# Performance work log

Hardware: AMD Instinct MI355X
Metric: run time of the kernel (lower is better)

The kernel has to match this reference:

```python
import jax, jax.numpy as jnp
import numpy as np

NEG_SLOPE = 0.01  # torch nn.LeakyReLU default

def setup_inputs() -> dict:
    key = jax.random.key(0)
    k1, k2, k3, k4 = jax.random.split(key, 4)
    B, S, D, C = 4, 2048, 1024, 4096
    x = jax.random.normal(k1, (B, S, D), dtype=jnp.float32)
    # _reset_parameters: normal(mean=0, std=0.1)
    atten_emb = jax.random.normal(k2, (C, D), dtype=jnp.float32) * 0.1
    # nn.Linear default init ~ U(-1/sqrt(D), 1/sqrt(D))
    bound = 1.0 / np.sqrt(D)
    W = jax.random.uniform(k3, (C, D), dtype=jnp.float32, minval=-bound, maxval=bound)
    b = jax.random.uniform(k4, (C,), dtype=jnp.float32, minval=-bound, maxval=bound)
    return {"x": x, "atten_emb": atten_emb, "W": W, "b": b}

def reference(x, atten_emb, W, b):
    shape = x.shape
    xf = x.reshape(-1, shape[-1])                      # [N, D]
    # dropout p=0.0 -> identity (eval path)
    scores = jnp.einsum('nd,cd->nc', xf, atten_emb)    # [N, C]
    probs = jax.nn.softmax(scores, axis=-1)
    xf = xf + probs @ atten_emb                        # residual with attended codebook
    y = xf.reshape(shape)
    y = jnp.einsum('...d,cd->...c', y, W) + b          # Linear
    return jnp.where(y >= 0, y, NEG_SLOPE * y)         # LeakyReLU
```

## Files before the change

kernel.cpp:

```cpp
#include <hip/hip_runtime.h>
#include <hip/hip_bf16.h>
#include <stdint.h>

typedef unsigned short u16;
typedef __attribute__((ext_vector_type(8))) short short8;
typedef __attribute__((ext_vector_type(4))) float f32x4;

__device__ inline u16 f2bf(float f) {
  union { float f; uint32_t u; } x; x.f = f;
  uint32_t r = (x.u + 0x7FFFu + ((x.u >> 16) & 1u)) >> 16;
  return (u16)r;
}

__device__ inline void async_load16(const void* g, void* l) {
  __builtin_amdgcn_global_load_lds(
      (const __attribute__((address_space(1))) void*)g,
      (__attribute__((address_space(3))) void*)l, 16, 0, 0);
}

__device__ inline void xcd_remap(int& bx, int& by) {
  int gx = gridDim.x;
  int nwg = gx * gridDim.y;
  int flat = by * gx + bx;
  int swz = (flat & 7) * (nwg >> 3) + (flat >> 3);
  bx = swz % gx;
  by = swz / gx;
}

__global__ __launch_bounds__(256) void f32_to_bf16_k(
    const float* __restrict__ in, u16* __restrict__ out, int n4) {
  int i = blockIdx.x * 256 + threadIdx.x;
  if (i >= n4) return;
  float4 v = reinterpret_cast<const float4*>(in)[i];
  ushort4 o;
  o.x = f2bf(v.x); o.y = f2bf(v.y); o.z = f2bf(v.z); o.w = f2bf(v.w);
  reinterpret_cast<ushort4*>(out)[i] = o;
}

__global__ __launch_bounds__(256) void transpose_f32_bf16_k(
    const float* __restrict__ in, u16* __restrict__ out_t,
    u16* __restrict__ out_nt, int R, int Cc) {
  __shared__ float tile[32][33];
  int tx = threadIdx.x & 31;
  int ty = threadIdx.x >> 5;
  int c = blockIdx.x * 32 + tx;
#pragma unroll
  for (int j = 0; j < 4; j++) {
    int r = blockIdx.y * 32 + ty + j * 8;
    float v = in[(size_t)r * Cc + c];
    tile[ty + j * 8][tx] = v;
    out_nt[(size_t)r * Cc + c] = f2bf(v);
  }
  __syncthreads();
  int rr = blockIdx.y * 32 + tx;
#pragma unroll
  for (int j = 0; j < 4; j++) {
    int cc = blockIdx.x * 32 + ty + j * 8;
    out_t[(size_t)cc * R + rr] = f2bf(tile[tx][ty + j * 8]);
  }
}

__global__ __launch_bounds__(256) void softmax_rows_k(
    const float* __restrict__ S, u16* __restrict__ P, int C) {
  const float4* src = reinterpret_cast<const float4*>(S + (size_t)blockIdx.x * C);
  ushort4* dst = reinterpret_cast<ushort4*>(P + (size_t)blockIdx.x * 2 * C);
  const int t = threadIdx.x;
  float4 v[4];
  float mx = -3.4e38f;
#pragma unroll
  for (int j = 0; j < 4; j++) {
    v[j] = src[j * 256 + t];
    mx = fmaxf(mx, fmaxf(fmaxf(v[j].x, v[j].y), fmaxf(v[j].z, v[j].w)));
  }
#pragma unroll
  for (int i = 1; i < 64; i <<= 1) mx = fmaxf(mx, __shfl_xor(mx, i));
  __shared__ float red[8];
  if ((t & 63) == 0) red[t >> 6] = mx;
  __syncthreads();
  mx = fmaxf(fmaxf(red[0], red[1]), fmaxf(red[2], red[3]));
  float e[16];
  float sum = 0.f;
#pragma unroll
  for (int j = 0; j < 4; j++) {
    e[j * 4 + 0] = __expf(v[j].x - mx);
    e[j * 4 + 1] = __expf(v[j].y - mx);
    e[j * 4 + 2] = __expf(v[j].z - mx);
    e[j * 4 + 3] = __expf(v[j].w - mx);
    sum += (e[j * 4 + 0] + e[j * 4 + 1]) + (e[j * 4 + 2] + e[j * 4 + 3]);
  }
#pragma unroll
  for (int i = 1; i < 64; i <<= 1) sum += __shfl_xor(sum, i);
  if ((t & 63) == 0) red[4 + (t >> 6)] = sum;
  __syncthreads();
  sum = (red[4] + red[5]) + (red[6] + red[7]);
  float inv = 1.0f / sum;
#pragma unroll
  for (int j = 0; j < 4; j++) {
    ushort4 o;
    o.x = f2bf(e[j * 4 + 0] * inv);
    o.y = f2bf(e[j * 4 + 1] * inv);
    o.z = f2bf(e[j * 4 + 2] * inv);
    o.w = f2bf(e[j * 4 + 3] * inv);
    dst[j * 256 + t] = o;
  }
}

template <int EPI>
__global__ __launch_bounds__(512, 2) void gemm_bt256p_k(
    const u16* __restrict__ A, const u16* __restrict__ B,
    int M, int N, int K, int lda,
    float* __restrict__ outF, u16* __restrict__ outBF,
    const float* __restrict__ aux) {
  __shared__ u16 sA[2][256 * 64];
  __shared__ u16 sB[2][256 * 64];

  int bx = blockIdx.x, by = blockIdx.y;
  xcd_remap(bx, by);
  const int mBase = by * 256, nBase = bx * 256;

  const int tid = threadIdx.x;
  const int l = tid & 63;
  const int w = tid >> 6;
  const int wr = w >> 2;
  const int wc = w & 3;
  const int fr = l & 15;
  const int kc4 = l >> 4;

  f32x4 acc[8][4];
#pragma unroll
  for (int m = 0; m < 8; m++)
#pragma unroll
    for (int n = 0; n < 4; n++) acc[m][n] = (f32x4)0.f;

  auto stageA = [&](int buf, int k0, int h) {
#pragma unroll
    for (int q = 0; q < 2; q++) {
      int cc = q * 512 + tid;
      int lr = cc >> 3, cs = cc & 7;
      int gr = (lr & 63) | (h << 6) | ((lr >> 6) << 7);
      int kc = (cs ^ (gr & 7)) << 3;
      async_load16(&A[(size_t)(mBase + gr) * lda + k0 + kc],
                   &sA[buf][gr * 64 + cs * 8]);
    }
  };
  auto stageB = [&](int buf, int k0, int v) {
#pragma unroll
    for (int q = 0; q < 2; q++) {
      int cc = q * 512 + tid;
      int lr = cc >> 3, cs = cc & 7;
      int gr = (lr & 31) | (v << 5) | ((lr >> 5) << 6);
      int kc = (cs ^ (gr & 7)) << 3;
      async_load16(&B[(size_t)(nBase + gr) * K + k0 + kc],
                   &sB[buf][gr * 64 + cs * 8]);
    }
  };

  const int nt = K / 64;
  stageA(0, 0, 0); stageB(0, 0, 0); stageB(0, 0, 1); stageA(0, 0, 1);

  short8 a[4][2], b0[2][2], b1[2][2];

  for (int T = 0; T < nt - 1; ++T) {
    const int buf = T & 1;
    const u16* sa = sA[buf];
    const u16* sb = sB[buf];
    const int k1 = (T + 1) * 64;

    asm volatile("s_waitcnt vmcnt(4)" ::: "memory");
    __builtin_amdgcn_s_barrier();
#pragma unroll
    for (int mm = 0; mm < 4; mm++) {
      int row = wr * 128 + mm * 16 + fr;
#pragma unroll
      for (int kk = 0; kk < 2; kk++)
        a[mm][kk] = *reinterpret_cast<const short8*>(
            &sa[row * 64 + (((kk * 4 + kc4) ^ (row & 7)) << 3)]);
    }
#pragma unroll
    for (int nn = 0; nn < 2; nn++) {
      int row = wc * 64 + nn * 16 + fr;
#pragma unroll
      for (int kk = 0; kk < 2; kk++)
        b0[nn][kk] = *reinterpret_cast<const short8*>(
            &sb[row * 64 + (((kk * 4 + kc4) ^ (row & 7)) << 3)]);
    }
    stageA(buf ^ 1, k1, 0);
    __builtin_amdgcn_s_setprio(1);
#pragma unroll
    for (int mm = 0; mm < 4; mm++)
#pragma unroll
      for (int nn = 0; nn < 2; nn++)
#pragma unroll
        for (int kk = 0; kk < 2; kk++)
          acc[mm][nn] = __builtin_amdgcn_mfma_f32_16x16x32_bf16(
              a[mm][kk], b0[nn][kk], acc[mm][nn], 0, 0, 0);
    __builtin_amdgcn_s_setprio(0);

    asm volatile("s_waitcnt vmcnt(4)" ::: "memory");
    __builtin_amdgcn_s_barrier();
#pragma unroll
    for (int nn = 0; nn < 2; nn++) {
      int row = wc * 64 + 32 + nn * 16 + fr;
#pragma unroll
      for (int kk = 0; kk < 2; kk++)
        b1[nn][kk] = *reinterpret_cast<const short8*>(
            &sb[row * 64 + (((kk * 4 + kc4) ^ (row & 7)) << 3)]);
    }
    stageB(buf ^ 1, k1, 0);
    __builtin_amdgcn_s_setprio(1);
#pragma unroll
    for (int mm = 0; mm < 4; mm++)
#pragma unroll
      for (int nn = 0; nn < 2; nn++)
#pragma unroll
        for (int kk = 0; kk < 2; kk++)
          acc[mm][2 + nn] = __builtin_amdgcn_mfma_f32_16x16x32_bf16(
              a[mm][kk], b1[nn][kk], acc[mm][2 + nn], 0, 0, 0);
    __builtin_amdgcn_s_setprio(0);

    asm volatile("s_waitcnt vmcnt(4)" ::: "memory");
    __builtin_amdgcn_s_barrier();
#pragma unroll
    for (int mm = 0; mm < 4; mm++) {
      int row = wr * 128 + 64 + mm * 16 + fr;
#pragma unroll
      for (int kk = 0; kk < 2; kk++)
        a[mm][kk] = *reinterpret_cast<const short8*>(
            &sa[row * 64 + (((kk * 4 + kc4) ^ (row & 7)) << 3)]);
    }
    stageB(buf ^ 1, k1, 1);
    __builtin_amdgcn_s_setprio(1);
#pragma unroll
    for (int mm = 0; mm < 4; mm++)
#pragma unroll
      for (int nn = 0; nn < 2; nn++)
#pragma unroll
        for (int kk = 0; kk < 2; kk++)
          acc[4 + mm][2 + nn] = __builtin_amdgcn_mfma_f32_16x16x32_bf16(
              a[mm][kk], b1[nn][kk], acc[4 + mm][2 + nn], 0, 0, 0);
    __builtin_amdgcn_s_setprio(0);

    stageA(buf ^ 1, k1, 1);
    __builtin_amdgcn_s_setprio(1);
#pragma unroll
    for (int mm = 0; mm < 4; mm++)
#pragma unroll
      for (int nn = 0; nn < 2; nn++)
#pragma unroll
        for (int kk = 0; kk < 2; kk++)
          acc[4 + mm][nn] = __builtin_amdgcn_mfma_f32_16x16x32_bf16(
              a[mm][kk], b0[nn][kk], acc[4 + mm][nn], 0, 0, 0);
    __builtin_amdgcn_s_setprio(0);
  }

  {
    const int buf = (nt - 1) & 1;
    const u16* sa = sA[buf];
    const u16* sb = sB[buf];

    asm volatile("s_waitcnt vmcnt(4)" ::: "memory");
    __builtin_amdgcn_s_barrier();
#pragma unroll
    for (int mm = 0; mm < 4; mm++) {
      int row = wr * 128 + mm * 16 + fr;
#pragma unroll
      for (int kk = 0; kk < 2; kk++)
        a[mm][kk] = *reinterpret_cast<const short8*>(
            &sa[row * 64 + (((kk * 4 + kc4) ^ (row & 7)) << 3)]);
    }
#pragma unroll
    for (int nn = 0; nn < 2; nn++) {
      int row = wc * 64 + nn * 16 + fr;
#pragma unroll
      for (int kk = 0; kk < 2; kk++)
        b0[nn][kk] = *reinterpret_cast<const short8*>(
            &sb[row * 64 + (((kk * 4 + kc4) ^ (row & 7)) << 3)]);
    }
    __builtin_amdgcn_s_setprio(1);
#pragma unroll
    for (int mm = 0; mm < 4; mm++)
#pragma unroll
      for (int nn = 0; nn < 2; nn++)
#pragma unroll
        for (int kk = 0; kk < 2; kk++)
          acc[mm][nn] = __builtin_amdgcn_mfma_f32_16x16x32_bf16(
              a[mm][kk], b0[nn][kk], acc[mm][nn], 0, 0, 0);
    __builtin_amdgcn_s_setprio(0);

    asm volatile("s_waitcnt vmcnt(2)" ::: "memory");
    __builtin_amdgcn_s_barrier();
#pragma unroll
    for (int nn = 0; nn < 2; nn++) {
      int row = wc * 64 + 32 + nn * 16 + fr;
#pragma unroll
      for (int kk = 0; kk < 2; kk++)
        b1[nn][kk] = *reinterpret_cast<const short8*>(
            &sb[row * 64 + (((kk * 4 + kc4) ^ (row & 7)) << 3)]);
    }
    __builtin_amdgcn_s_setprio(1);
#pragma unroll
    for (int mm = 0; mm < 4; mm++)
#pragma unroll
      for (int nn = 0; nn < 2; nn++)
#pragma unroll
        for (int kk = 0; kk < 2; kk++)
          acc[mm][2 + nn] = __builtin_amdgcn_mfma_f32_16x16x32_bf16(
              a[mm][kk], b1[nn][kk], acc[mm][2 + nn], 0, 0, 0);
    __builtin_amdgcn_s_setprio(0);

    asm volatile("s_waitcnt vmcnt(0)" ::: "memory");
    __builtin_amdgcn_s_barrier();
#pragma unroll
    for (int mm = 0; mm < 4; mm++) {
      int row = wr * 128 + 64 + mm * 16 + fr;
#pragma unroll
      for (int kk = 0; kk < 2; kk++)
        a[mm][kk] = *reinterpret_cast<const short8*>(
            &sa[row * 64 + (((kk * 4 + kc4) ^ (row & 7)) << 3)]);
    }
    __builtin_amdgcn_s_setprio(1);
#pragma unroll
    for (int mm = 0; mm < 4; mm++)
#pragma unroll
      for (int nn = 0; nn < 2; nn++)
#pragma unroll
        for (int kk = 0; kk < 2; kk++)
          acc[4 + mm][2 + nn] = __builtin_amdgcn_mfma_f32_16x16x32_bf16(
              a[mm][kk], b1[nn][kk], acc[4 + mm][2 + nn], 0, 0, 0);
    __builtin_amdgcn_s_setprio(0);

    __builtin_amdgcn_s_setprio(1);
#pragma unroll
    for (int mm = 0; mm < 4; mm++)
#pragma unroll
      for (int nn = 0; nn < 2; nn++)
#pragma unroll
        for (int kk = 0; kk < 2; kk++)
          acc[4 + mm][nn] = __builtin_amdgcn_mfma_f32_16x16x32_bf16(
              a[mm][kk], b0[nn][kk], acc[4 + mm][nn], 0, 0, 0);
    __builtin_amdgcn_s_setprio(0);
  }

#pragma unroll
  for (int m = 0; m < 8; m++) {
#pragma unroll
    for (int n = 0; n < 4; n++) {
      int col = nBase + wc * 64 + n * 16 + fr;
#pragma unroll
      for (int r = 0; r < 4; r++) {
        int row = mBase + wr * 128 + m * 16 + (l >> 4) * 4 + r;
        size_t o = (size_t)row * N + col;
        float v = acc[m][n][r];
        if (EPI == 0) {
          outF[o] = v;
        } else if (EPI == 1) {
          outBF[o] = f2bf(v + aux[o]);
        } else {
          v += aux[col];
          outF[o] = (v >= 0.f) ? v : 0.01f * v;
        }
      }
    }
  }
}

template <int EPI>
__global__ __launch_bounds__(256, 2) void gemm_bt_k(
    const u16* __restrict__ A, const u16* __restrict__ B,
    int M, int N, int K, int lda,
    float* __restrict__ outF, u16* __restrict__ outBF,
    const float* __restrict__ aux) {
  __shared__ u16 sA[4][128 * 32];
  __shared__ u16 sB[4][128 * 32];

  int bx = blockIdx.x, by = blockIdx.y;
  xcd_remap(bx, by);
  const int mBase = by * 128;
  const int nBase = bx * 128;

  const int tid = threadIdx.x;
  const int l = tid & 63;
  const int w = tid >> 6;
  const int wr = w >> 1;
  const int wc = w & 1;
  const int fr = l & 15;
  const int kc4 = l >> 4;

  f32x4 acc[4][4];
#pragma unroll
  for (int m = 0; m < 4; m++)
#pragma unroll
    for (int n = 0; n < 4; n++) acc[m][n] = (f32x4)0.f;

  auto stage = [&](int slot, int k0) {
#pragma unroll
    for (int q = 0; q < 2; q++) {
      int c = q * 256 + tid;
      int row = c >> 2;
      int cs = c & 3;
      int kc = ((cs ^ ((row >> 1) & 3)) << 3);
      async_load16(&A[(size_t)(mBase + row) * lda + k0 + kc], &sA[slot][c * 8]);
      async_load16(&B[(size_t)(nBase + row) * K + k0 + kc], &sB[slot][c * 8]);
    }
  };

  const int nt = K / 32;
  stage(0, 0); stage(1, 32); stage(2, 64); stage(3, 96);

  for (int t = 0; t < nt; ++t) {
    asm volatile("s_waitcnt vmcnt(12)" ::: "memory");
    __builtin_amdgcn_s_barrier();

    const u16* sa = sA[t & 3];
    const u16* sb = sB[t & 3];
    short8 af[4], bf[4];
#pragma unroll
    for (int m = 0; m < 4; m++) {
      int row = wr * 64 + m * 16 + fr;
      af[m] = *reinterpret_cast<const short8*>(
          &sa[row * 32 + ((kc4 ^ ((row >> 1) & 3)) << 3)]);
    }
#pragma unroll
    for (int n = 0; n < 4; n++) {
      int row = wc * 64 + n * 16 + fr;
      bf[n] = *reinterpret_cast<const short8*>(
          &sb[row * 32 + ((kc4 ^ ((row >> 1) & 3)) << 3)]);
    }

    __builtin_amdgcn_s_setprio(1);
#pragma unroll
    for (int m = 0; m < 4; m++)
#pragma unroll
      for (int n = 0; n < 4; n++)
        acc[m][n] = __builtin_amdgcn_mfma_f32_16x16x32_bf16(af[m], bf[n], acc[m][n], 0, 0, 0);
    __builtin_amdgcn_s_setprio(0);

    asm volatile("s_waitcnt lgkmcnt(0)" ::: "memory");
    __builtin_amdgcn_s_barrier();
    if (t + 4 < nt) stage((t + 4) & 3, (t + 4) * 32);
  }

#pragma unroll
  for (int m = 0; m < 4; m++) {
#pragma unroll
    for (int n = 0; n < 4; n++) {
      int col = nBase + wc * 64 + n * 16 + fr;
#pragma unroll
      for (int r = 0; r < 4; r++) {
        int row = mBase + wr * 64 + m * 16 + (l >> 4) * 4 + r;
        size_t o = (size_t)row * N + col;
        float v = acc[m][n][r];
        if (EPI == 0) {
          outF[o] = v;
        } else if (EPI == 1) {
          outBF[o] = f2bf(v + aux[o]);
        } else {
          v += aux[col];
          outF[o] = (v >= 0.f) ? v : 0.01f * v;
        }
      }
    }
  }
}

extern "C" void kernel_launch(void* const* d_in, const int* in_sizes, int n_in,
                              void* d_out, int out_size, void* d_ws, size_t ws_size,
                              hipStream_t stream) {
  const float* x = (const float*)d_in[0];
  const float* E = (const float*)d_in[1];
  const float* W = (const float*)d_in[2];
  const float* bias = (const float*)d_in[3];

  const int C = in_sizes[3];
  const int D = in_sizes[1] / C;
  const int Mrows = in_sizes[0] / D;

  char* p = (char*)d_ws;
  u16* xbf = (u16*)p;   p += (size_t)Mrows * D * 2;
  u16* Ebf = (u16*)p;   p += (size_t)C * D * 2;
  u16* Etbf = (u16*)p;  p += (size_t)C * D * 2;
  u16* Wbf = (u16*)p;   p += (size_t)C * D * 2;
  u16* x2bf = (u16*)p;  p += (size_t)Mrows * D * 2;
  float* scores = (float*)p;
  u16* probs = (u16*)scores + C;

  {
    int n4 = Mrows * D / 4;
    f32_to_bf16_k<<<(n4 + 255) / 256, 256, 0, stream>>>(x, xbf, n4);
  }
  {
    int n4 = C * D / 4;
    f32_to_bf16_k<<<(n4 + 255) / 256, 256, 0, stream>>>(W, Wbf, n4);
  }
  transpose_f32_bf16_k<<<dim3(D / 32, C / 32), 256, 0, stream>>>(E, Etbf, Ebf, C, D);

  gemm_bt256p_k<0><<<dim3(C / 256, Mrows / 256), 512, 0, stream>>>(
      xbf, Ebf, Mrows, C, D, D, scores, nullptr, nullptr);

  softmax_rows_k<<<Mrows, 256, 0, stream>>>(scores, probs, C);

  gemm_bt_k<1><<<dim3(D / 128, Mrows / 128), 256, 0, stream>>>(
      probs, Etbf, Mrows, D, C, 2 * C, nullptr, x2bf, x);

  gemm_bt256p_k<2><<<dim3(C / 256, Mrows / 256), 512, 0, stream>>>(
      x2bf, Wbf, Mrows, C, D, D, (float*)d_out, nullptr, bias);
}
```

Before: 438.6 us.

## Fuse prep conversions into one kernel and retile probs@E GEMM to 256x128

```diff
diff --git a/kernel.cpp b/kernel.cpp
--- a/kernel.cpp
+++ b/kernel.cpp
@@ -27,36 +27,58 @@
   by = swz / gx;
 }
 
-__global__ __launch_bounds__(256) void f32_to_bf16_k(
-    const float* __restrict__ in, u16* __restrict__ out, int n4) {
-  int i = blockIdx.x * 256 + threadIdx.x;
-  if (i >= n4) return;
-  float4 v = reinterpret_cast<const float4*>(in)[i];
-  ushort4 o;
-  o.x = f2bf(v.x); o.y = f2bf(v.y); o.z = f2bf(v.z); o.w = f2bf(v.w);
-  reinterpret_cast<ushort4*>(out)[i] = o;
-}
-
-__global__ __launch_bounds__(256) void transpose_f32_bf16_k(
-    const float* __restrict__ in, u16* __restrict__ out_t,
-    u16* __restrict__ out_nt, int R, int Cc) {
+__global__ __launch_bounds__(256) void prep_k(
+    const float* __restrict__ x, u16* __restrict__ xbf, int n4x, int nbx,
+    const float* __restrict__ W, u16* __restrict__ Wbf, int n4w, int nbw,
+    const float* __restrict__ E, u16* __restrict__ Ebf, u16* __restrict__ Etbf,
+    int R, int Cc) {
   __shared__ float tile[32][33];
-  int tx = threadIdx.x & 31;
-  int ty = threadIdx.x >> 5;
-  int c = blockIdx.x * 32 + tx;
-#pragma unroll
-  for (int j = 0; j < 4; j++) {
-    int r = blockIdx.y * 32 + ty + j * 8;
-    float v = in[(size_t)r * Cc + c];
-    tile[ty + j * 8][tx] = v;
-    out_nt[(size_t)r * Cc + c] = f2bf(v);
-  }
-  __syncthreads();
-  int rr = blockIdx.y * 32 + tx;
-#pragma unroll
-  for (int j = 0; j < 4; j++) {
-    int cc = blockIdx.x * 32 + ty + j * 8;
-    out_t[(size_t)cc * R + rr] = f2bf(tile[tx][ty + j * 8]);
+  const int b = blockIdx.x;
+  const int t = threadIdx.x;
+  if (b < nbx) {
+#pragma unroll
+    for (int j = 0; j < 4; j++) {
+      int i = b * 1024 + j * 256 + t;
+      if (i < n4x) {
+        float4 v = reinterpret_cast<const float4*>(x)[i];
+        ushort4 o;
+        o.x = f2bf(v.x); o.y = f2bf(v.y); o.z = f2bf(v.z); o.w = f2bf(v.w);
+        reinterpret_cast<ushort4*>(xbf)[i] = o;
+      }
+    }
+  } else if (b < nbx + nbw) {
+    int bb = b - nbx;
+#pragma unroll
+    for (int j = 0; j < 4; j++) {
+      int i = bb * 1024 + j * 256 + t;
+      if (i < n4w) {
+        float4 v = reinterpret_cast<const float4*>(W)[i];
+        ushort4 o;
+        o.x = f2bf(v.x); o.y = f2bf(v.y); o.z = f2bf(v.z); o.w = f2bf(v.w);
+        reinterpret_cast<ushort4*>(Wbf)[i] = o;
+      }
+    }
+  } else {
+    int bb = b - nbx - nbw;
+    int gbx = bb % (Cc / 32);
+    int gby = bb / (Cc / 32);
+    int tx = t & 31;
+    int ty = t >> 5;
+    int c = gbx * 32 + tx;
+#pragma unroll
+    for (int j = 0; j < 4; j++) {
+      int r = gby * 32 + ty + j * 8;
+      float v = E[(size_t)r * Cc + c];
+      tile[ty + j * 8][tx] = v;
+      Ebf[(size_t)r * Cc + c] = f2bf(v);
+    }
+    __syncthreads();
+    int rr = gby * 32 + tx;
+#pragma unroll
+    for (int j = 0; j < 4; j++) {
+      int cc = gbx * 32 + ty + j * 8;
+      Etbf[(size_t)cc * R + rr] = f2bf(tile[tx][ty + j * 8]);
+    }
   }
 }
 
@@ -353,8 +375,6 @@
         float v = acc[m][n][r];
         if (EPI == 0) {
           outF[o] = v;
-        } else if (EPI == 1) {
-          outBF[o] = f2bf(v + aux[o]);
         } else {
           v += aux[col];
           outF[o] = (v >= 0.f) ? v : 0.01f * v;
@@ -364,100 +384,184 @@
   }
 }
 
-template <int EPI>
-__global__ __launch_bounds__(256, 2) void gemm_bt_k(
+__global__ __launch_bounds__(512, 2) void gemm2_k(
     const u16* __restrict__ A, const u16* __restrict__ B,
     int M, int N, int K, int lda,
-    float* __restrict__ outF, u16* __restrict__ outBF,
-    const float* __restrict__ aux) {
-  __shared__ u16 sA[4][128 * 32];
-  __shared__ u16 sB[4][128 * 32];
+    u16* __restrict__ outBF, const float* __restrict__ aux) {
+  __shared__ u16 sA[2][256 * 64];
+  __shared__ u16 sB[2][128 * 64];
 
   int bx = blockIdx.x, by = blockIdx.y;
   xcd_remap(bx, by);
-  const int mBase = by * 128;
-  const int nBase = bx * 128;
+  const int mBase = by * 256, nBase = bx * 128;
 
   const int tid = threadIdx.x;
   const int l = tid & 63;
   const int w = tid >> 6;
-  const int wr = w >> 1;
-  const int wc = w & 1;
+  const int wr = w >> 2;
+  const int wc = w & 3;
   const int fr = l & 15;
   const int kc4 = l >> 4;
 
-  f32x4 acc[4][4];
-#pragma unroll
-  for (int m = 0; m < 4; m++)
-#pragma unroll
-    for (int n = 0; n < 4; n++) acc[m][n] = (f32x4)0.f;
-
-  auto stage = [&](int slot, int k0) {
+  f32x4 acc[8][2];
+#pragma unroll
+  for (int m = 0; m < 8; m++)
+#pragma unroll
+    for (int n = 0; n < 2; n++) acc[m][n] = (f32x4)0.f;
+
+  auto stageA = [&](int buf, int k0, int h) {
 #pragma unroll
     for (int q = 0; q < 2; q++) {
-      int c = q * 256 + tid;
-      int row = c >> 2;
-      int cs = c & 3;
-      int kc = ((cs ^ ((row >> 1) & 3)) << 3);
-      async_load16(&A[(size_t)(mBase + row) * lda + k0 + kc], &sA[slot][c * 8]);
-      async_load16(&B[(size_t)(nBase + row) * K + k0 + kc], &sB[slot][c * 8]);
+      int cc = q * 512 + tid;
+      int lr = cc >> 3, cs = cc & 7;
+      int gr = (lr & 63) | (h << 6) | ((lr >> 6) << 7);
+      int kc = (cs ^ (gr & 7)) << 3;
+      async_load16(&A[(size_t)(mBase + gr) * lda + k0 + kc],
+                   &sA[buf][gr * 64 + cs * 8]);
     }
   };
-
-  const int nt = K / 32;
-  stage(0, 0); stage(1, 32); stage(2, 64); stage(3, 96);
-
-  for (int t = 0; t < nt; ++t) {
-    asm volatile("s_waitcnt vmcnt(12)" ::: "memory");
-    __builtin_amdgcn_s_barrier();
-
-    const u16* sa = sA[t & 3];
-    const u16* sb = sB[t & 3];
-    short8 af[4], bf[4];
-#pragma unroll
-    for (int m = 0; m < 4; m++) {
-      int row = wr * 64 + m * 16 + fr;
-      af[m] = *reinterpret_cast<const short8*>(
-          &sa[row * 32 + ((kc4 ^ ((row >> 1) & 3)) << 3)]);
-    }
-#pragma unroll
-    for (int n = 0; n < 4; n++) {
-      int row = wc * 64 + n * 16 + fr;
-      bf[n] = *reinterpret_cast<const short8*>(
-          &sb[row * 32 + ((kc4 ^ ((row >> 1) & 3)) << 3)]);
-    }
-
-    __builtin_amdgcn_s_setprio(1);
-#pragma unroll
-    for (int m = 0; m < 4; m++)
-#pragma unroll
-      for (int n = 0; n < 4; n++)
-        acc[m][n] = __builtin_amdgcn_mfma_f32_16x16x32_bf16(af[m], bf[n], acc[m][n], 0, 0, 0);
-    __builtin_amdgcn_s_setprio(0);
-
-    asm volatile("s_waitcnt lgkmcnt(0)" ::: "memory");
-    __builtin_amdgcn_s_barrier();
-    if (t + 4 < nt) stage((t + 4) & 3, (t + 4) * 32);
-  }
-
-#pragma unroll
-  for (int m = 0; m < 4; m++) {
-#pragma unroll
-    for (int n = 0; n < 4; n++) {
-      int col = nBase + wc * 64 + n * 16 + fr;
+  auto stageB = [&](int buf, int k0) {
+#pragma unroll
+    for (int q = 0; q < 2; q++) {
+      int cc = q * 512 + tid;
+      int gr = cc >> 3, cs = cc & 7;
+      int kc = (cs ^ (gr & 7)) << 3;
+      async_load16(&B[(size_t)(nBase + gr) * K + k0 + kc],
+                   &sB[buf][gr * 64 + cs * 8]);
+    }
+  };
+
+  const int nt = K / 64;
+  stageA(0, 0, 0); stageB(0, 0); stageA(0, 0, 1);
+
+  short8 a[4][2], b[2][2];
+
+  for (int T = 0; T < nt - 1; ++T) {
+    const int buf = T & 1;
+    const u16* sa = sA[buf];
+    const u16* sb = sB[buf];
+    const int k1 = (T + 1) * 64;
+
+    asm volatile("s_waitcnt vmcnt(2)" ::: "memory");
+    __builtin_amdgcn_s_barrier();
+#pragma unroll
+    for (int mm = 0; mm < 4; mm++) {
+      int row = wr * 128 + mm * 16 + fr;
+#pragma unroll
+      for (int kk = 0; kk < 2; kk++)
+        a[mm][kk] = *reinterpret_cast<const short8*>(
+            &sa[row * 64 + (((kk * 4 + kc4) ^ (row & 7)) << 3)]);
+    }
+#pragma unroll
+    for (int nn = 0; nn < 2; nn++) {
+      int row = wc * 32 + nn * 16 + fr;
+#pragma unroll
+      for (int kk = 0; kk < 2; kk++)
+        b[nn][kk] = *reinterpret_cast<const short8*>(
+            &sb[row * 64 + (((kk * 4 + kc4) ^ (row & 7)) << 3)]);
+    }
+    stageA(buf ^ 1, k1, 0);
+    __builtin_amdgcn_s_setprio(1);
+#pragma unroll
+    for (int mm = 0; mm < 4; mm++)
+#pragma unroll
+      for (int nn = 0; nn < 2; nn++)
+#pragma unroll
+        for (int kk = 0; kk < 2; kk++)
+          acc[mm][nn] = __builtin_amdgcn_mfma_f32_16x16x32_bf16(
+              a[mm][kk], b[nn][kk], acc[mm][nn], 0, 0, 0);
+    __builtin_amdgcn_s_setprio(0);
+
+    asm volatile("s_waitcnt vmcnt(2)" ::: "memory");
+    __builtin_amdgcn_s_barrier();
+#pragma unroll
+    for (int mm = 0; mm < 4; mm++) {
+      int row = wr * 128 + 64 + mm * 16 + fr;
+#pragma unroll
+      for (int kk = 0; kk < 2; kk++)
+        a[mm][kk] = *reinterpret_cast<const short8*>(
+            &sa[row * 64 + (((kk * 4 + kc4) ^ (row & 7)) << 3)]);
+    }
+    stageB(buf ^ 1, k1);
+    stageA(buf ^ 1, k1, 1);
+    __builtin_amdgcn_s_setprio(1);
+#pragma unroll
+    for (int mm = 0; mm < 4; mm++)
+#pragma unroll
+      for (int nn = 0; nn < 2; nn++)
+#pragma unroll
+        for (int kk = 0; kk < 2; kk++)
+          acc[4 + mm][nn] = __builtin_amdgcn_mfma_f32_16x16x32_bf16(
+              a[mm][kk], b[nn][kk], acc[4 + mm][nn], 0, 0, 0);
+    __builtin_amdgcn_s_setprio(0);
+  }
+
+  {
+    const int buf = (nt - 1) & 1;
+    const u16* sa = sA[buf];
+    const u16* sb = sB[buf];
+
+    asm volatile("s_waitcnt vmcnt(2)" ::: "memory");
+    __builtin_amdgcn_s_barrier();
+#pragma unroll
+    for (int mm = 0; mm < 4; mm++) {
+      int row = wr * 128 + mm * 16 + fr;
+#pragma unroll
+      for (int kk = 0; kk < 2; kk++)
+        a[mm][kk] = *reinterpret_cast<const short8*>(
+            &sa[row * 64 + (((kk * 4 + kc4) ^ (row & 7)) << 3)]);
+    }
+#pragma unroll
+    for (int nn = 0; nn < 2; nn++) {
+      int row = wc * 32 + nn * 16 + fr;
+#pragma unroll
+      for (int kk = 0; kk < 2; kk++)
+        b[nn][kk] = *reinterpret_cast<const short8*>(
+            &sb[row * 64 + (((kk * 4 + kc4) ^ (row & 7)) << 3)]);
+    }
+    __builtin_amdgcn_s_setprio(1);
+#pragma unroll
+    for (int mm = 0; mm < 4; mm++)
+#pragma unroll
+      for (int nn = 0; nn < 2; nn++)
+#pragma unroll
+        for (int kk = 0; kk < 2; kk++)
+          acc[mm][nn] = __builtin_amdgcn_mfma_f32_16x16x32_bf16(
+              a[mm][kk], b[nn][kk], acc[mm][nn], 0, 0, 0);
+    __builtin_amdgcn_s_setprio(0);
+
+    asm volatile("s_waitcnt vmcnt(0)" ::: "memory");
+    __builtin_amdgcn_s_barrier();
+#pragma unroll
+    for (int mm = 0; mm < 4; mm++) {
+      int row = wr * 128 + 64 + mm * 16 + fr;
+#pragma unroll
+      for (int kk = 0; kk < 2; kk++)
+        a[mm][kk] = *reinterpret_cast<const short8*>(
+            &sa[row * 64 + (((kk * 4 + kc4) ^ (row & 7)) << 3)]);
+    }
+    __builtin_amdgcn_s_setprio(1);
+#pragma unroll
+    for (int mm = 0; mm < 4; mm++)
+#pragma unroll
+      for (int nn = 0; nn < 2; nn++)
+#pragma unroll
+        for (int kk = 0; kk < 2; kk++)
+          acc[4 + mm][nn] = __builtin_amdgcn_mfma_f32_16x16x32_bf16(
+              a[mm][kk], b[nn][kk], acc[4 + mm][nn], 0, 0, 0);
+    __builtin_amdgcn_s_setprio(0);
+  }
+
+#pragma unroll
+  for (int m = 0; m < 8; m++) {
+#pragma unroll
+    for (int n = 0; n < 2; n++) {
+      int col = nBase + wc * 32 + n * 16 + fr;
 #pragma unroll
       for (int r = 0; r < 4; r++) {
-        int row = mBase + wr * 64 + m * 16 + (l >> 4) * 4 + r;
+        int row = mBase + wr * 128 + m * 16 + (l >> 4) * 4 + r;
         size_t o = (size_t)row * N + col;
-        float v = acc[m][n][r];
-        if (EPI == 0) {
-          outF[o] = v;
-        } else if (EPI == 1) {
-          outBF[o] = f2bf(v + aux[o]);
-        } else {
-          v += aux[col];
-          outF[o] = (v >= 0.f) ? v : 0.01f * v;
-        }
+        outBF[o] = f2bf(acc[m][n][r] + aux[o]);
       }
     }
   }
@@ -485,22 +589,22 @@
   u16* probs = (u16*)scores + C;
 
   {
-    int n4 = Mrows * D / 4;
-    f32_to_bf16_k<<<(n4 + 255) / 256, 256, 0, stream>>>(x, xbf, n4);
-  }
-  {
-    int n4 = C * D / 4;
-    f32_to_bf16_k<<<(n4 + 255) / 256, 256, 0, stream>>>(W, Wbf, n4);
-  }
-  transpose_f32_bf16_k<<<dim3(D / 32, C / 32), 256, 0, stream>>>(E, Etbf, Ebf, C, D);
+    int n4x = Mrows * D / 4;
+    int n4w = C * D / 4;
+    int nbx = (n4x + 1023) / 1024;
+    int nbw = (n4w + 1023) / 1024;
+    int nbt = (D / 32) * (C / 32);
+    prep_k<<<nbx + nbw + nbt, 256, 0, stream>>>(
+        x, xbf, n4x, nbx, W, Wbf, n4w, nbw, E, Ebf, Etbf, C, D);
+  }
 
   gemm_bt256p_k<0><<<dim3(C / 256, Mrows / 256), 512, 0, stream>>>(
       xbf, Ebf, Mrows, C, D, D, scores, nullptr, nullptr);
 
   softmax_rows_k<<<Mrows, 256, 0, stream>>>(scores, probs, C);
 
-  gemm_bt_k<1><<<dim3(D / 128, Mrows / 128), 256, 0, stream>>>(
-      probs, Etbf, Mrows, D, C, 2 * C, nullptr, x2bf, x);
+  gemm2_k<<<dim3(D / 128, Mrows / 256), 512, 0, stream>>>(
+      probs, Etbf, Mrows, D, C, 2 * C, x2bf, x);
 
   gemm_bt256p_k<2><<<dim3(C / 256, Mrows / 256), 512, 0, stream>>>(
       x2bf, Wbf, Mrows, C, D, D, (float*)d_out, nullptr, bias);
```

New measurement: 416.9 us. 4.9% less time.
